# Kernel tuning notes

Hardware: AMD Instinct MI355X
Metric: run time of the kernel (lower is better)

The kernel has to match this reference:

```python
import jax, jax.numpy as jnp
import numpy as np

DEPTH = 6; HEADS = 6; DIM = 384; HD = DIM // HEADS
WS = 14; WINDOW_BLOCKS = (0, 1, 3, 4)
IMG = 512; PATCH = 16; GRID = IMG // PATCH        # 32x32 token grid
PRE_GRID = 14                                      # 224 // 16 pretrain grid
SCALE = HD ** -0.5


def layer_norm(x, w, b, eps=1e-5):
    u = x.mean(-1, keepdims=True)
    s = ((x - u) ** 2).mean(-1, keepdims=True)
    return (x - u) / jnp.sqrt(s + eps) * w + b


def get_rel_pos(size, rel_pos):
    # q_size == k_size here; relative coords in [0, 2*size-2]
    coords = jnp.arange(size)[:, None] - jnp.arange(size)[None, :] + (size - 1)
    return rel_pos[coords]  # (size, size, HD)


def attention(x, qkv_w, qkv_b, proj_w, proj_b, rel_h, rel_w):
    B, H, W, C = x.shape
    N = H * W
    qkv = (x.reshape(B, N, C) @ qkv_w.T + qkv_b).reshape(B, N, 3, HEADS, HD)
    qkv = jnp.moveaxis(qkv, 2, 0).transpose(0, 1, 3, 2, 4)  # (3,B,h,N,d)
    q, k, v = qkv[0], qkv[1], qkv[2]
    attn = jnp.einsum('bhqd,bhkd->bhqk', q * SCALE, k)
    # decomposed relative position bias (ViTDet add_decomposed_rel_pos)
    Rh = get_rel_pos(H, rel_h)  # (H,H,d)
    Rw = get_rel_pos(W, rel_w)  # (W,W,d)
    rq = q.reshape(B, HEADS, H, W, HD)
    bias_h = jnp.einsum('bnhwc,hkc->bnhwk', rq, Rh)  # (B,h,H,W,H)
    bias_w = jnp.einsum('bnhwc,wkc->bnhwk', rq, Rw)  # (B,h,H,W,W)
    attn = (attn.reshape(B, HEADS, H, W, H, W)
            + bias_h[..., :, None] + bias_w[..., None, :]).reshape(B, HEADS, N, N)
    attn = jax.nn.softmax(attn, axis=-1)
    out = jnp.einsum('bhqk,bhkd->bhqd', attn, v)
    out = out.transpose(0, 2, 1, 3).reshape(B, H, W, C)
    return out @ proj_w.T + proj_b


def window_partition(x, ws):
    B, H, W, C = x.shape
    pad_h = (ws - H % ws) % ws
    pad_w = (ws - W % ws) % ws
    x = jnp.pad(x, ((0, 0), (0, pad_h), (0, pad_w), (0, 0)))
    Hp, Wp = H + pad_h, W + pad_w
    x = x.reshape(B, Hp // ws, ws, Wp // ws, ws, C)
    x = x.transpose(0, 1, 3, 2, 4, 5).reshape(-1, ws, ws, C)
    return x, Hp, Wp


def window_unpartition(win, ws, Hp, Wp, H, W):
    B = win.shape[0] // ((Hp // ws) * (Wp // ws))
    x = win.reshape(B, Hp // ws, Wp // ws, ws, ws, -1)
    x = x.transpose(0, 1, 3, 2, 4, 5).reshape(B, Hp, Wp, -1)
    return x[:, :H, :W]


def block(x, p, windowed):
    shortcut = x
    x = layer_norm(x, p['n1w'], p['n1b'])
    if windowed:
        H, W = x.shape[1], x.shape[2]
        x, Hp, Wp = window_partition(x, WS)
    x = attention(x, p['qw'], p['qb'], p['pw'], p['pb'], p['rh'], p['rw'])
    if windowed:
        x = window_unpartition(x, WS, Hp, Wp, H, W)
    x = shortcut + x
    h = layer_norm(x, p['n2w'], p['n2b'])
    h = jax.nn.gelu(h @ p['f1w'].T + p['f1b'], approximate=False)
    return x + h @ p['f2w'].T + p['f2b']


def vit_forward(x, patch_w, patch_b, pos_embed, norm1_w, norm1_b, qkv_w, qkv_b,
                proj_w, proj_b, norm2_w, norm2_b, fc1_w, fc1_b, fc2_w, fc2_b,
                rel_pos_h, rel_pos_w):
    y = jax.lax.conv_general_dilated(
        x, patch_w, (PATCH, PATCH), 'VALID',
        dimension_numbers=('NCHW', 'OIHW', 'NCHW'))
    y = y.transpose(0, 2, 3, 1) + patch_b  # (B, GRID, GRID, DIM)
    # abs pos embed: bicubic resize from pretrain 14x14 grid to 32x32
    pos = pos_embed.reshape(1, PRE_GRID, PRE_GRID, DIM)
    pos = jax.image.resize(pos, (1, GRID, GRID, DIM), 'bicubic')
    y = y + pos
    for i in range(DEPTH):
        windowed = i in WINDOW_BLOCKS
        L = 2 * WS - 1 if windowed else 2 * GRID - 1
        p = dict(n1w=norm1_w[i], n1b=norm1_b[i], qw=qkv_w[i], qb=qkv_b[i],
                 pw=proj_w[i], pb=proj_b[i], rh=rel_pos_h[i, :L], rw=rel_pos_w[i, :L],
                 n2w=norm2_w[i], n2b=norm2_b[i], f1w=fc1_w[i], f1b=fc1_b[i],
                 f2w=fc2_w[i], f2b=fc2_b[i])
        y = block(y, p, windowed)
    return y.transpose(0, 3, 1, 2)  # (B, DIM, GRID, GRID) 'last_feat'


def setup_inputs() -> dict:
    key = jax.random.key(0)
    ks = jax.random.split(key, 10)
    B = 4
    std = 0.02
    f32 = jnp.float32
    return {
        'x': jax.random.normal(ks[0], (B, 3, IMG, IMG), f32),
        'patch_w': jax.random.normal(ks[1], (DIM, 3, PATCH, PATCH), f32) * 0.05,
        'patch_b': jnp.zeros((DIM,), f32),
        'pos_embed': jax.random.normal(ks[2], (1, PRE_GRID * PRE_GRID, DIM), f32) * std,
        'norm1_w': jnp.ones((DEPTH, DIM), f32),
        'norm1_b': jnp.zeros((DEPTH, DIM), f32),
        'qkv_w': jax.random.normal(ks[3], (DEPTH, 3 * DIM, DIM), f32) * std,
        'qkv_b': jnp.zeros((DEPTH, 3 * DIM), f32),
        'proj_w': jax.random.normal(ks[4], (DEPTH, DIM, DIM), f32) * std,
        'proj_b': jnp.zeros((DEPTH, DIM), f32),
        'norm2_w': jnp.ones((DEPTH, DIM), f32),
        'norm2_b': jnp.zeros((DEPTH, DIM), f32),
        'fc1_w': jax.random.normal(ks[5], (DEPTH, 4 * DIM, DIM), f32) * std,
        'fc1_b': jnp.zeros((DEPTH, 4 * DIM), f32),
        'fc2_w': jax.random.normal(ks[6], (DEPTH, DIM, 4 * DIM), f32) * std,
        'fc2_b': jnp.zeros((DEPTH, DIM), f32),
        'rel_pos_h': jax.random.normal(ks[7], (DEPTH, 2 * GRID - 1, HD), f32) * std,
        'rel_pos_w': jax.random.normal(ks[8], (DEPTH, 2 * GRID - 1, HD), f32) * std,
    }


def reference(x, patch_w, patch_b, pos_embed, norm1_w, norm1_b, qkv_w, qkv_b,
              proj_w, proj_b, norm2_w, norm2_b, fc1_w, fc1_b, fc2_w, fc2_b,
              rel_pos_h, rel_pos_w):
    return vit_forward(x, patch_w, patch_b, pos_embed, norm1_w, norm1_b, qkv_w, qkv_b,
                       proj_w, proj_b, norm2_w, norm2_b, fc1_w, fc1_b, fc2_w, fc2_b,
                       rel_pos_h, rel_pos_w)
```

## Files before the change

### kernel.cpp

```cpp
#include <hip/hip_runtime.h>
#include <hip/hip_bf16.h>
#include <math.h>

#define B_SZ 4
#define DIM 384
#define HEADS 6
#define HD 64
#define NTOK 4096
#define WS 14
#define NWIN 36
#define WTOK 196

typedef unsigned short u16;
typedef __bf16 bf16_t;
typedef bf16_t bf16x8 __attribute__((ext_vector_type(8)));
typedef float f32x4 __attribute__((ext_vector_type(4)));

__device__ __forceinline__ float bf2f(unsigned u) { return __uint_as_float(u << 16); }
__device__ __forceinline__ u16 f2bf(float f) {
    unsigned u = __float_as_uint(f);
    unsigned r = (u + 0x7fffu + ((u >> 16) & 1u)) >> 16;
    return (u16)r;
}
__device__ __forceinline__ unsigned pk2bf(float a, float b) {
    __hip_bfloat162 h = __float22bfloat162_rn(make_float2(a, b));
    unsigned r; __builtin_memcpy(&r, &h, 4); return r;
}

__device__ __forceinline__ void ldsload16(const u16* g, u16* l) {
    __builtin_amdgcn_global_load_lds(
        (const __attribute__((address_space(1))) unsigned int*)g,
        (__attribute__((address_space(3))) unsigned int*)l, 16, 0, 0);
}

__device__ __forceinline__ int swz(int r) { return (r ^ (r >> 2)) & 3; }

__device__ inline float cubic_keys(float x) {
    x = fabsf(x);
    if (x <= 1.f) return ((1.5f * x - 2.5f) * x) * x + 1.f;
    if (x < 2.f)  return ((-0.5f * x + 2.5f) * x - 4.f) * x + 2.f;
    return 0.f;
}

__global__ __launch_bounds__(256) void setup_kernel(
        const float* __restrict__ p0, const float* __restrict__ p1,
        const float* __restrict__ p2, const float* __restrict__ p3,
        const float* __restrict__ p4, const float* __restrict__ p5,
        u16* __restrict__ wb, const float* __restrict__ pe,
        float* __restrict__ posr, const float* __restrict__ x,
        u16* __restrict__ col) {
    int i = (blockIdx.x * 256 + threadIdx.x) * 4;
    if (i < 10918656) {
        const float* s; int off;
        if      (i <   294912) { s = p0; off = 0; }
        else if (i <  2949120) { s = p1; off = 294912; }
        else if (i <  3833856) { s = p2; off = 2949120; }
        else if (i <  7372800) { s = p3; off = 3833856; }
        else if (i < 10911744) { s = p4; off = 7372800; }
        else                   { s = p5; off = 10911744; }
        float4 v = *(const float4*)(s + (i - off));
        u16 o[4] = { f2bf(v.x), f2bf(v.y), f2bf(v.z), f2bf(v.w) };
        *(uint2*)(wb + i) = *(const uint2*)o;
        return;
    }
    i -= 10918656;
    if (i < 393216) {
        int c = i % 384;
        int g = i / 384;
        int gy = g / 32, gx = g % 32;
        float wy[14], wx[14];
        float sy = (gy + 0.5f) * (14.f / 32.f) - 0.5f;
        float sx = (gx + 0.5f) * (14.f / 32.f) - 0.5f;
        float toty = 0.f, totx = 0.f;
        #pragma unroll
        for (int k = 0; k < 14; ++k) {
            wy[k] = cubic_keys(sy - (float)k); toty += wy[k];
            wx[k] = cubic_keys(sx - (float)k); totx += wx[k];
        }
        float4 acc = {0.f, 0.f, 0.f, 0.f};
        #pragma unroll 1
        for (int iy = 0; iy < 14; ++iy) {
            if (wy[iy] == 0.f) continue;
            float4 row = {0.f, 0.f, 0.f, 0.f};
            for (int ix = 0; ix < 14; ++ix) {
                if (wx[ix] == 0.f) continue;
                float4 pv = *(const float4*)(pe + (iy * 14 + ix) * 384 + c);
                row.x += wx[ix] * pv.x; row.y += wx[ix] * pv.y;
                row.z += wx[ix] * pv.z; row.w += wx[ix] * pv.w;
            }
            acc.x += wy[iy] * row.x; acc.y += wy[iy] * row.y;
            acc.z += wy[iy] * row.z; acc.w += wy[iy] * row.w;
        }
        float inv = 1.f / (toty * totx);
        acc.x *= inv; acc.y *= inv; acc.z *= inv; acc.w *= inv;
        *(float4*)(posr + i) = acc;
        return;
    }
    i -= 393216;
    if (i < 3145728) {
        int kk = i % 768;
        int p  = i / 768;
        int b  = p / 1024;
        int ph = (p % 1024) / 32;
        int pw = p % 32;
        int c = kk / 256;
        int r = kk % 256;
        int ii = r / 16, j = r % 16;
        float4 v = *(const float4*)(x + (size_t)b * 3 * 512 * 512 +
                                    (size_t)c * 512 * 512 +
                                    (size_t)(ph * 16 + ii) * 512 + (pw * 16 + j));
        u16 o[4] = { f2bf(v.x), f2bf(v.y), f2bf(v.z), f2bf(v.w) };
        *(uint2*)(col + i) = *(const uint2*)o;
    }
}

__global__ __launch_bounds__(256) void ln_kernel(const float* __restrict__ y,
        const float* __restrict__ lw, const float* __restrict__ lb,
        u16* __restrict__ lnout)
{
    int tok = blockIdx.x * 4 + (threadIdx.x >> 6);
    int t = threadIdx.x & 63;
    size_t base = (size_t)tok * 384;
    float v[6];
    float s = 0.f;
    #pragma unroll
    for (int i = 0; i < 6; ++i) {
        v[i] = y[base + t + 64 * i]; s += v[i];
    }
    #pragma unroll
    for (int off = 32; off > 0; off >>= 1) s += __shfl_xor(s, off);
    float mean = s * (1.f / 384.f);
    float vs = 0.f;
    #pragma unroll
    for (int i = 0; i < 6; ++i) { float d = v[i] - mean; vs += d * d; }
    #pragma unroll
    for (int off = 32; off > 0; off >>= 1) vs += __shfl_xor(vs, off);
    float inv = rsqrtf(vs * (1.f / 384.f) + 1e-5f);
    u16* orow = lnout + base;
    #pragma unroll
    for (int i = 0; i < 6; ++i) {
        int c = t + 64 * i;
        orow[c] = f2bf((v[i] - mean) * inv * lw[c] + lb[c]);
    }
}

__global__ __launch_bounds__(256) void out_transpose(const float* __restrict__ y,
        float* __restrict__ outT)
{
    __shared__ float T[64][65];
    int c0 = blockIdx.x * 64, m0 = blockIdx.y * 64;
    int t = threadIdx.x;
    int cl = t & 63, wv = t >> 6;
    #pragma unroll
    for (int r = 0; r < 16; ++r) {
        int ml = wv * 16 + r;
        T[ml][cl] = y[(size_t)(m0 + ml) * 384 + c0 + cl];
    }
    __syncthreads();
    int b = m0 >> 10, g0 = m0 & 1023;
    int gl = t & 63;
    #pragma unroll
    for (int r = 0; r < 16; ++r) {
        int ccl = wv * 16 + r;
        outT[((size_t)(b * 384 + c0 + ccl)) * 1024 + g0 + gl] = T[gl][ccl];
    }
}

__global__ __launch_bounds__(256) void mfma_gemm4(
        const u16* __restrict__ A, const u16* __restrict__ Wt,
        const float* __restrict__ bias,
        u16* __restrict__ outb,
        int M, int N, int K, int act)
{
    __shared__ u16 As[2][8192];
    __shared__ u16 Bs[2][4096];
    int t = threadIdx.x;
    int lane = t & 63, wave = t >> 6;
    int wm = (wave >> 1) * 64, wn = (wave & 1) * 32;
    int m0 = blockIdx.y * 128, n0 = blockIdx.x * 64;

    int r0 = t >> 2,        c0 = ((t & 3) ^ swz(t >> 2)) * 8;
    int r1 = 64 + (t >> 2), c1 = ((t & 3) ^ swz(64 + (t >> 2))) * 8;
    const u16* a0 = A + (size_t)(m0 + r0) * K + c0;
    const u16* a1 = A + (size_t)(m0 + r1) * K + c1;
    const u16* b0 = Wt + (size_t)(n0 + r0) * K + c0;

    auto stage = [&](int k0, int buf) {
        ldsload16(a0 + k0,      &As[buf][wave * 512]);
        ldsload16(a1 + k0,      &As[buf][2048 + wave * 512]);
        ldsload16(b0 + k0,      &Bs[buf][wave * 512]);
        ldsload16(a0 + k0 + 32, &As[buf][4096 + wave * 512]);
        ldsload16(a1 + k0 + 32, &As[buf][6144 + wave * 512]);
        ldsload16(b0 + k0 + 32, &Bs[buf][2048 + wave * 512]);
    };

    f32x4 acc[4][2] = {};
    int row_a = wm + (lane & 15);
    int row_b = wn + (lane & 15);
    int lq = lane >> 4;
    int nchunks = K / 64;

    stage(0, 0);
    __syncthreads();

    for (int ci = 0; ci < nchunks; ++ci) {
        int p = ci & 1;
        bool pref = (ci + 1 < nchunks);
        if (pref) stage((ci + 1) * 64, 1 - p);
        #pragma unroll
        for (int hf = 0; hf < 2; ++hf) {
            bf16x8 af[4], bfr[2];
            #pragma unroll
            for (int i = 0; i < 4; ++i) {
                int r = row_a + i * 16;
                af[i] = *(const bf16x8*)&As[p][hf * 4096 + r * 32 + ((lq ^ swz(r)) * 8)];
            }
            #pragma unroll
            for (int j = 0; j < 2; ++j) {
                int r = row_b + j * 16;
                bfr[j] = *(const bf16x8*)&Bs[p][hf * 2048 + r * 32 + ((lq ^ swz(r)) * 8)];
            }
            #pragma unroll
            for (int i = 0; i < 4; ++i)
                #pragma unroll
                for (int j = 0; j < 2; ++j)
                    acc[i][j] = __builtin_amdgcn_mfma_f32_16x16x32_bf16(
                        af[i], bfr[j], acc[i][j], 0, 0, 0);
        }
        if (pref) __syncthreads();
    }

    int colq = lane & 15, rowq = (lane >> 4) * 4;
    #pragma unroll
    for (int i = 0; i < 4; ++i) {
        #pragma unroll
        for (int rr = 0; rr < 4; ++rr) {
            int m = m0 + wm + i * 16 + rowq + rr;
            size_t mo = (size_t)m * N;
            #pragma unroll
            for (int j = 0; j < 2; ++j) {
                int n = n0 + wn + j * 16 + colq;
                float v = acc[i][j][rr] + bias[n];
                if (act)  v = 0.5f * v * (1.f + erff(v * 0.70710678118654752f));
                outb[mo + n] = f2bf(v);
            }
        }
    }
}

__global__ __launch_bounds__(256) void mfma_gemm32(
        const u16* __restrict__ A, const u16* __restrict__ Wt,
        const float* __restrict__ bias, const float* __restrict__ posr,
        float* __restrict__ y, int addy, int M, int N, int K)
{
    __shared__ u16 As[2][4096];
    __shared__ u16 Bs[2][2048];
    int t = threadIdx.x;
    int lane = t & 63, wave = t >> 6;
    int wm = (wave >> 1) * 32, wn = (wave & 1) * 16;
    int m0 = blockIdx.y * 64, n0 = blockIdx.x * 32;

    int r0 = t >> 2, c0 = ((t & 3) ^ swz(t >> 2)) * 8;
    const u16* a0 = A + (size_t)(m0 + r0) * K + c0;
    int tb = t & 127;
    int rb = tb >> 2, cb = ((tb & 3) ^ swz(tb >> 2)) * 8;
    const u16* b0 = Wt + (size_t)(n0 + rb) * K + cb;

    auto stage = [&](int k0, int buf) {
        ldsload16(a0 + k0,      &As[buf][wave * 512]);
        ldsload16(a0 + k0 + 32, &As[buf][2048 + wave * 512]);
        if (wave < 2) ldsload16(b0 + k0,      &Bs[buf][wave * 512]);
        else          ldsload16(b0 + k0 + 32, &Bs[buf][1024 + (wave - 2) * 512]);
    };

    f32x4 acc[2] = {};
    int row_a = wm + (lane & 15);
    int row_b = wn + (lane & 15);
    int lq = lane >> 4;
    int nchunks = K / 64;

    stage(0, 0);
    __syncthreads();

    for (int ci = 0; ci < nchunks; ++ci) {
        int p = ci & 1;
        bool pref = (ci + 1 < nchunks);
        if (pref) stage((ci + 1) * 64, 1 - p);
        #pragma unroll
        for (int hf = 0; hf < 2; ++hf) {
            bf16x8 af[2], bf0;
            #pragma unroll
            for (int i = 0; i < 2; ++i) {
                int r = row_a + i * 16;
                af[i] = *(const bf16x8*)&As[p][hf * 2048 + r * 32 + ((lq ^ swz(r)) * 8)];
            }
            {
                int r = row_b;
                bf0 = *(const bf16x8*)&Bs[p][hf * 1024 + r * 32 + ((lq ^ swz(r)) * 8)];
            }
            #pragma unroll
            for (int i = 0; i < 2; ++i)
                acc[i] = __builtin_amdgcn_mfma_f32_16x16x32_bf16(
                    af[i], bf0, acc[i], 0, 0, 0);
        }
        if (pref) __syncthreads();
    }

    int colq = lane & 15, rowq = (lane >> 4) * 4;
    #pragma unroll
    for (int i = 0; i < 2; ++i) {
        #pragma unroll
        for (int rr = 0; rr < 4; ++rr) {
            int m = m0 + wm + i * 16 + rowq + rr;
            size_t mo = (size_t)m * N;
            int n = n0 + wn + colq;
            float v = acc[i][rr] + bias[n];
            if (posr) v += posr[(size_t)(m & 1023) * 384 + n];
            if (addy) v += y[mo + n];
            y[mo + n] = v;
        }
    }
}

__global__ __launch_bounds__(256) void mfma_gemm32b(
        const u16* __restrict__ A, const u16* __restrict__ Wt,
        const float* __restrict__ bias, u16* __restrict__ outb,
        int M, int N, int K)
{
    __shared__ u16 As[2][4096];
    __shared__ u16 Bs[2][2048];
    int t = threadIdx.x;
    int lane = t & 63, wave = t >> 6;
    int wm = (wave >> 1) * 32, wn = (wave & 1) * 16;
    int m0 = blockIdx.y * 64, n0 = blockIdx.x * 32;

    int r0 = t >> 2, c0 = ((t & 3) ^ swz(t >> 2)) * 8;
    const u16* a0 = A + (size_t)(m0 + r0) * K + c0;
    int tb = t & 127;
    int rb = tb >> 2, cb = ((tb & 3) ^ swz(tb >> 2)) * 8;
    const u16* b0 = Wt + (size_t)(n0 + rb) * K + cb;

    auto stage = [&](int k0, int buf) {
        ldsload16(a0 + k0,      &As[buf][wave * 512]);
        ldsload16(a0 + k0 + 32, &As[buf][2048 + wave * 512]);
        if (wave < 2) ldsload16(b0 + k0,      &Bs[buf][wave * 512]);
        else          ldsload16(b0 + k0 + 32, &Bs[buf][1024 + (wave - 2) * 512]);
    };

    f32x4 acc[2] = {};
    int row_a = wm + (lane & 15);
    int row_b = wn + (lane & 15);
    int lq = lane >> 4;
    int nchunks = K / 64;

    stage(0, 0);
    __syncthreads();

    for (int ci = 0; ci < nchunks; ++ci) {
        int p = ci & 1;
        bool pref = (ci + 1 < nchunks);
        if (pref) stage((ci + 1) * 64, 1 - p);
        #pragma unroll
        for (int hf = 0; hf < 2; ++hf) {
            bf16x8 af[2], bf0;
            #pragma unroll
            for (int i = 0; i < 2; ++i) {
                int r = row_a + i * 16;
                af[i] = *(const bf16x8*)&As[p][hf * 2048 + r * 32 + ((lq ^ swz(r)) * 8)];
            }
            {
                int r = row_b;
                bf0 = *(const bf16x8*)&Bs[p][hf * 1024 + r * 32 + ((lq ^ swz(r)) * 8)];
            }
            #pragma unroll
            for (int i = 0; i < 2; ++i)
                acc[i] = __builtin_amdgcn_mfma_f32_16x16x32_bf16(
                    af[i], bf0, acc[i], 0, 0, 0);
        }
        if (pref) __syncthreads();
    }

    int colq = lane & 15, rowq = (lane >> 4) * 4;
    #pragma unroll
    for (int i = 0; i < 2; ++i) {
        #pragma unroll
        for (int rr = 0; rr < 4; ++rr) {
            int m = m0 + wm + i * 16 + rowq + rr;
            size_t mo = (size_t)m * N;
            int n = n0 + wn + colq;
            outb[mo + n] = f2bf(acc[i][rr] + bias[n]);
        }
    }
}

template<int N, int W>
__global__ __launch_bounds__(256) void attn_mfma(const u16* __restrict__ qkv,
        const u16* __restrict__ qkb, const float* __restrict__ rh,
        const float* __restrict__ rw, u16* __restrict__ outb,
        float* __restrict__ opart, float* __restrict__ lpart)
{
    constexpr int JS = (W == 32) ? 64 : 32;
    constexpr int L  = (W == 32) ? 63 : 27;
    constexpr int CTR = W - 1;
    constexpr int KSPAN = (W == 32) ? 512 : 224;
    constexpr int NKT = KSPAN / 32;
    __shared__ u16 KV[11776];
    __shared__ u16 bhl[64 * 66];
    __shared__ u16 bwl[64 * 66];
    __shared__ u16 Qt[64 * 66];
    __shared__ unsigned kofs[224];

    u16* Pb = KV + 9216;
    u16* Rt = KV;

    int t = threadIdx.x, lane = t & 63, wave = t >> 6;
    int quad = lane >> 4, l15 = lane & 15;
    int uh = blockIdx.x, qb0 = blockIdx.y * 64;
    int z = (W == 32) ? blockIdx.z : 0;
    int kstart = z * KSPAN;
    int h = uh % HEADS, u = uh / HEADS;
    size_t tbase = (size_t)u * 1024;
    int wb_ = u / 9, wr = u - wb_ * 9;
    int wy = wr / 3, wx = wr - wy * 3;

    auto tok14 = [&](int iy, int ix) -> const u16* {
        int gy = wy * WS + iy, gx = wx * WS + ix;
        if (gy < 32 && gx < 32)
            return qkv + (size_t)(wb_ * 1024 + gy * 32 + gx) * 1152;
        return qkb;
    };
    auto rowptr = [&](int lq2) -> const u16* {
        if constexpr (W == 32) {
            return qkv + (tbase + lq2) * 1152;
        } else {
            int iy = lq2 / WS, ix = lq2 - iy * WS;
            return tok14(iy, ix);
        }
    };

    {
        int q = t & 63, ch0 = (t >> 6) * 16;
        int qc = qb0 + q; if (qc >= N) qc = N - 1;
        const u16* qp = rowptr(qc) + h * 64 + ch0;
        uint4 a = *(const uint4*)qp;
        uint4 b = *(const uint4*)(qp + 8);
        u16 vals[16];
        *(uint4*)vals = a; *(uint4*)(vals + 8) = b;
        #pragma unroll
        for (int c = 0; c < 16; ++c)
            Qt[(ch0 + c) * 66 + q] = ((qb0 + q) < N) ? vals[c] : (u16)0;
    }

    if constexpr (W != 32) {
        if (t < 224) {
            int kh = t / WS;
            kofs[t] = (unsigned)kh | ((unsigned)(t - kh * WS) << 16);
        }
    }

    for (int idx = t; idx < JS * 16; idx += 256) {
        int table = (idx >= JS * 8) ? 1 : 0;
        int id2 = idx & (JS * 8 - 1);
        int j = id2 >> 3, cc0 = (id2 & 7) * 8;
        const float* tab = table ? rw : rh;
        u16 tmp[8];
        if (j < L) {
            const float* src = tab + (size_t)j * 64 + cc0;
            #pragma unroll
            for (int c = 0; c < 8; ++c) tmp[c] = f2bf(src[c]);
        } else {
            #pragma unroll
            for (int c = 0; c < 8; ++c) tmp[c] = 0;
        }
        *(uint4*)&Rt[table * JS * 72 + j * 72 + cc0] = *(uint4*)tmp;
    }
    __syncthreads();

    {
        int tb0 = (W == 32) ? 0 : (wave >> 1);
        int ntb = (W == 32) ? 2 : 1;
        int jt  = (W == 32) ? wave : (wave & 1);
        for (int tt = 0; tt < ntb; ++tt) {
            int table = tb0 + tt;
            const u16* Rtt = Rt + table * JS * 72;
            bf16x8 af0 = *(const bf16x8*)&Rtt[(jt * 16 + l15) * 72 + quad * 8];
            bf16x8 af1 = *(const bf16x8*)&Rtt[(jt * 16 + l15) * 72 + 32 + quad * 8];
            u16* dst = table ? bwl : bhl;
            #pragma unroll
            for (int qt = 0; qt < 4; ++qt) {
                bf16x8 qf0, qf1;
                u16* p0 = (u16*)&qf0; u16* p1 = (u16*)&qf1;
                #pragma unroll
                for (int zz = 0; zz < 8; ++zz) {
                    p0[zz] = Qt[(quad * 8 + zz) * 66 + qt * 16 + l15];
                    p1[zz] = Qt[(32 + quad * 8 + zz) * 66 + qt * 16 + l15];
                }
                f32x4 acc = {};
                acc = __builtin_amdgcn_mfma_f32_16x16x32_bf16(af0, qf0, acc, 0, 0, 0);
                acc = __builtin_amdgcn_mfma_f32_16x16x32_bf16(af1, qf1, acc, 0, 0, 0);
                #pragma unroll
                for (int r = 0; r < 4; ++r)
                    dst[(qt * 16 + l15) * 66 + jt * 16 + quad * 4 + r] = f2bf(acc[r]);
            }
        }
    }
    __syncthreads();

    int skey = (wave * 64 + lane) >> 3;
    int sc8  = ((wave * 64 + lane) & 7) ^ (skey & 7);
    int vkey = t & 31, vch0 = (t >> 5) * 8;
    int siy = 0, six = 0, viy = 0, vix = 0;
    if constexpr (W != 32) {
        int k0 = kstart + skey;
        siy = k0 / WS; six = k0 - siy * WS;
        int k1 = kstart + vkey;
        viy = k1 / WS; vix = k1 - viy * WS;
    }
    auto adv = [](int& iy, int& ix) { ix += 4; iy += 2; if (ix >= WS) { ix -= WS; ++iy; } };

    {
        const u16* kp = (W == 32) ? qkv + (tbase + kstart + skey) * 1152
                                  : tok14(siy, six);
        ldsload16(kp + 384 + h * 64 + sc8 * 8, KV + wave * 512);
        const u16* vp = (W == 32) ? qkv + (tbase + kstart + vkey) * 1152
                                  : tok14(viy, vix);
        uint4 vv = *(const uint4*)(vp + 768 + h * 64 + vch0);
        u16 tmp[8]; *(uint4*)tmp = vv;
        u16* vdst = KV + 4096;
        #pragma unroll
        for (int c = 0; c < 8; ++c) vdst[(vch0 + c) * 40 + vkey] = tmp[c];
        if constexpr (W != 32) { adv(siy, six); adv(viy, vix); }
    }

    bf16x8 qf[2];
    #pragma unroll
    for (int hc = 0; hc < 2; ++hc) {
        u16* qv = (u16*)&qf[hc];
        #pragma unroll
        for (int j = 0; j < 8; ++j)
            qv[j] = Qt[(hc * 32 + quad * 8 + j) * 66 + wave * 16 + l15];
    }
    int qme = wave * 16 + l15;
    bool wactive = (W == 32) ? true : ((qb0 + wave * 16) < N);
    int qq = qb0 + qme; if (qq >= N) qq = N - 1;
    int qh = qq / W, qw = qq - qh * W;
    int qh13 = qh + CTR, qw13 = qw + CTR;
    float bwreg[2][4];
    if constexpr (W == 32) {
        #pragma unroll
        for (int kc2 = 0; kc2 < 2; ++kc2)
            #pragma unroll
            for (int r = 0; r < 4; ++r) {
                int keyl = kc2 * 16 + quad * 4 + r;
                bwreg[kc2][r] = bf2f(bwl[qme * 66 + (qw - keyl + CTR)]);
            }
    }

    f32x4 of[4] = {};
    float lsum = 0.f;
    __syncthreads();

    for (int kt = 0; kt < NKT; ++kt) {
        int kb = kstart + kt * 32;
        int p = kt & 1;
        const u16* ksp = KV + p * 2048;
        const u16* vtp = KV + 4096 + p * 2560;
        bool pref = (kt + 1 < NKT);
        uint4 vpref;
        if (pref) {
            const u16* kp = (W == 32) ? qkv + (tbase + kb + 32 + skey) * 1152
                                      : tok14(siy, six);
            ldsload16(kp + 384 + h * 64 + sc8 * 8, KV + (1 - p) * 2048 + wave * 512);
            const u16* vp = (W == 32) ? qkv + (tbase + kb + 32 + vkey) * 1152
                                      : tok14(viy, vix);
            vpref = *(const uint4*)(vp + 768 + h * 64 + vch0);
            if constexpr (W != 32) { adv(siy, six); adv(viy, vix); }
        }

        if (wactive) {
            f32x4 st[2] = {};
            #pragma unroll
            for (int hc = 0; hc < 2; ++hc) {
                #pragma unroll
                for (int kc2 = 0; kc2 < 2; ++kc2) {
                    int key = kc2 * 16 + l15;
                    int c8 = hc * 4 + quad;
                    int pp = key * 8 + (c8 ^ (key & 7));
                    bf16x8 kf = *(const bf16x8*)&ksp[pp * 8];
                    st[kc2] = __builtin_amdgcn_mfma_f32_16x16x32_bf16(
                        kf, qf[hc], st[kc2], 0, 0, 0);
                }
            }
            float bh_t = 0.f;
            if constexpr (W == 32) bh_t = bf2f(bhl[qme * 66 + (qh - (kb >> 5) + CTR)]);
            #pragma unroll
            for (int kc2 = 0; kc2 < 2; ++kc2) {
                float pv4[4];
                #pragma unroll
                for (int r = 0; r < 4; ++r) {
                    int keyl = kc2 * 16 + quad * 4 + r;
                    float pv;
                    if constexpr (W == 32) {
                        float b = bh_t + bwreg[kc2][r];
                        pv = __expf(fmaf(st[kc2][r], 0.125f, b));
                    } else {
                        unsigned ko = kofs[kb + keyl];
                        float b = bf2f(bhl[qme * 66 + qh13 - (int)(ko & 0xffffu)]) +
                                  bf2f(bwl[qme * 66 + qw13 - (int)(ko >> 16)]);
                        pv = __expf(fmaf(st[kc2][r], 0.125f, b));
                        if (kb + keyl >= N) pv = 0.f;
                    }
                    lsum += pv;
                    pv4[r] = pv;
                }
                uint2 pk;
                pk.x = pk2bf(pv4[0], pv4[1]);
                pk.y = pk2bf(pv4[2], pv4[3]);
                *(uint2*)&Pb[wave * 640 + l15 * 40 + kc2 * 16 + quad * 4] = pk;
            }
            bf16x8 pf = *(const bf16x8*)&Pb[wave * 640 + l15 * 40 + quad * 8];
            #pragma unroll
            for (int ca = 0; ca < 4; ++ca) {
                bf16x8 vf = *(const bf16x8*)&vtp[(ca * 16 + l15) * 40 + quad * 8];
                of[ca] = __builtin_amdgcn_mfma_f32_16x16x32_bf16(
                    vf, pf, of[ca], 0, 0, 0);
            }
        }

        if (pref) {
            u16 tmp[8]; *(uint4*)tmp = vpref;
            u16* vdst = KV + 4096 + (1 - p) * 2560;
            #pragma unroll
            for (int c = 0; c < 8; ++c) vdst[(vch0 + c) * 40 + vkey] = tmp[c];
            __syncthreads();
        }
    }

    lsum += __shfl_xor(lsum, 16);
    lsum += __shfl_xor(lsum, 32);
    int q = qb0 + qme;
    if constexpr (W == 32) {
        size_t ridx = (size_t)z * 24576 + (size_t)uh * 1024 + q;
        float* op = opart + ridx * 64;
        #pragma unroll
        for (int ca = 0; ca < 4; ++ca)
            *(float4*)&op[ca * 16 + quad * 4] = (float4){of[ca][0], of[ca][1],
                                                         of[ca][2], of[ca][3]};
        if (quad == 0) lpart[ridx] = lsum;
    } else {
        float inv = 1.f / lsum;
        if (q < N) {
            int iy = q / WS, ix = q - iy * WS;
            int gy = wy * WS + iy, gx = wx * WS + ix;
            if (gy >= 32 || gx >= 32) return;
            u16* op = outb + (size_t)(wb_ * 1024 + gy * 32 + gx) * 384 + h * 64;
            #pragma unroll
            for (int ca = 0; ca < 4; ++ca) {
                uint2 pk;
                pk.x = pk2bf(of[ca][0] * inv, of[ca][1] * inv);
                pk.y = pk2bf(of[ca][2] * inv, of[ca][3] * inv);
                *(uint2*)&op[ca * 16 + quad * 4] = pk;
            }
        }
    }
}

__global__ __launch_bounds__(256) void attn_merge_kernel(const float* __restrict__ O,
        const float* __restrict__ Lp, u16* __restrict__ attb)
{
    int gi = blockIdx.x * 256 + threadIdx.x;
    int idx = gi >> 4;
    int ch = (gi & 15) * 4;
    float4 o0 = *(const float4*)&O[(size_t)idx * 64 + ch];
    float4 o1 = *(const float4*)&O[((size_t)24576 + idx) * 64 + ch];
    float inv = 1.f / (Lp[idx] + Lp[24576 + idx]);
    int uh = idx >> 10, q = idx & 1023;
    int u = uh / 6, h = uh - u * 6;
    uint2 pk;
    pk.x = pk2bf((o0.x + o1.x) * inv, (o0.y + o1.y) * inv);
    pk.y = pk2bf((o0.z + o1.z) * inv, (o0.w + o1.w) * inv);
    *(uint2*)(attb + ((size_t)(u * 1024 + q)) * 384 + h * 64 + ch) = pk;
}

static inline void launch_gemm(const u16* A, const u16* W, const float* bias,
                               u16* outb, int M, int N, int K, int act,
                               hipStream_t s) {
    dim3 g(N / 64, M / 128, 1);
    mfma_gemm4<<<g, 256, 0, s>>>(A, W, bias, outb, M, N, K, act);
}

static inline void launch_gemm32(const u16* A, const u16* W, const float* bias,
                                 const float* posr, float* y, int addy,
                                 int M, int N, int K, hipStream_t s) {
    dim3 g(N / 32, M / 64, 1);
    mfma_gemm32<<<g, 256, 0, s>>>(A, W, bias, posr, y, addy, M, N, K);
}

static inline void launch_gemm32b(const u16* A, const u16* W, const float* bias,
                                  u16* outb, int M, int N, int K, hipStream_t s) {
    dim3 g(N / 32, M / 64, 1);
    mfma_gemm32b<<<g, 256, 0, s>>>(A, W, bias, outb, M, N, K);
}

extern "C" void kernel_launch(void* const* d_in, const int* in_sizes, int n_in,
                              void* d_out, int out_size, void* d_ws, size_t ws_size,
                              hipStream_t stream) {
    const float* x      = (const float*)d_in[0];
    const float* patchw = (const float*)d_in[1];
    const float* patchb = (const float*)d_in[2];
    const float* pos    = (const float*)d_in[3];
    const float* n1w    = (const float*)d_in[4];
    const float* n1b    = (const float*)d_in[5];
    const float* qkvw   = (const float*)d_in[6];
    const float* qkvb   = (const float*)d_in[7];
    const float* pw     = (const float*)d_in[8];
    const float* pb     = (const float*)d_in[9];
    const float* n2w    = (const float*)d_in[10];
    const float* n2b    = (const float*)d_in[11];
    const float* f1w    = (const float*)d_in[12];
    const float* f1b    = (const float*)d_in[13];
    const float* f2w    = (const float*)d_in[14];
    const float* f2b    = (const float*)d_in[15];
    const float* rph    = (const float*)d_in[16];
    const float* rpw    = (const float*)d_in[17];
    float* out = (float*)d_out;

    float* y   = (float*)d_ws;
    u16* attb  = (u16*)(y + 1572864);
    u16* mlpb  = attb + 1572864;
    u16* lnb   = mlpb + 6291456;
    u16* qkvx  = lnb + 1572864;
    u16* rsrv  = qkvx + 4718592;
    u16* wb    = rsrv + 7864320;
    float* posr = (float*)(wb + 10918656);

    u16* colb  = rsrv;
    float* Opart   = (float*)mlpb;
    float* Lpart   = (float*)lnb;

    u16* wb_patch = wb;
    u16* wb_qkv   = wb + 294912;
    u16* wb_pw    = wb + 2949120;
    u16* wb_f1    = wb + 3833856;
    u16* wb_f2    = wb + 7372800;
    u16* wqb      = wb + 10911744;

    setup_kernel<<<(14457600 / 4 + 255) / 256, 256, 0, stream>>>(
        patchw, qkvw, pw, f1w, f2w, qkvb, wb, pos, posr, x, colb);

    launch_gemm32(colb, wb_patch, patchb, posr, y, 0, NTOK, 384, 768, stream);
    ln_kernel<<<1024, 256, 0, stream>>>(y, n1w, n1b, lnb);

    for (int i = 0; i < 6; ++i) {
        bool windowed = (i == 0 || i == 1 || i == 3 || i == 4);
        const float* rh = rph + (size_t)i * 63 * 64;
        const float* rw = rpw + (size_t)i * 63 * 64;
        launch_gemm32b(lnb, wb_qkv + (size_t)i * 442368, qkvb + i * 1152,
                       qkvx, NTOK, 1152, 384, stream);
        if (windowed) {
            attn_mfma<WTOK, WS><<<dim3(NWIN * HEADS, 4, 1), 256, 0, stream>>>(
                qkvx, wqb + i * 1152, rh, rw, attb, nullptr, nullptr);
        } else {
            attn_mfma<1024, 32><<<dim3(B_SZ * HEADS, 16, 2), 256, 0, stream>>>(
                qkvx, wqb + i * 1152, rh, rw, nullptr, Opart, Lpart);
            attn_merge_kernel<<<1536, 256, 0, stream>>>(Opart, Lpart, attb);
        }
        launch_gemm32(attb, wb_pw + (size_t)i * 147456, pb + i * 384,
                      nullptr, y, 1, NTOK, 384, 384, stream);
        ln_kernel<<<1024, 256, 0, stream>>>(y, n2w + i * 384, n2b + i * 384, lnb);
        launch_gemm(lnb, wb_f1 + (size_t)i * 589824, f1b + i * 1536,
                    mlpb, NTOK, 1536, 384, 1, stream);
        launch_gemm32(mlpb, wb_f2 + (size_t)i * 589824, f2b + i * 384,
                      nullptr, y, 1, NTOK, 384, 1536, stream);
        if (i < 5)
            ln_kernel<<<1024, 256, 0, stream>>>(y, n1w + (i + 1) * 384,
                                                n1b + (i + 1) * 384, lnb);
        else
            out_transpose<<<dim3(6, 64), 256, 0, stream>>>(y, out);
    }
}
```

Measured before the change: 684.1 us.

## Remap GEMM blocks across XCDs, widen QKV tile, deepen K-chunk in gemm32

```diff
diff --git a/kernel.cpp b/kernel.cpp
--- a/kernel.cpp
+++ b/kernel.cpp
@@ -34,6 +34,18 @@
 }
 
 __device__ __forceinline__ int swz(int r) { return (r ^ (r >> 2)) & 3; }
+
+__device__ __forceinline__ void xcd_remap(int& bx, int& by) {
+    int nwg = gridDim.x * gridDim.y;
+    int id = blockIdx.y * gridDim.x + blockIdx.x;
+    if ((nwg & 7) == 0) {
+        int nid = (id & 7) * (nwg >> 3) + (id >> 3);
+        by = nid / gridDim.x;
+        bx = nid - by * gridDim.x;
+    } else {
+        bx = blockIdx.x; by = blockIdx.y;
+    }
+}
 
 __device__ inline float cubic_keys(float x) {
     x = fabsf(x);
@@ -177,7 +189,9 @@
     int t = threadIdx.x;
     int lane = t & 63, wave = t >> 6;
     int wm = (wave >> 1) * 64, wn = (wave & 1) * 32;
-    int m0 = blockIdx.y * 128, n0 = blockIdx.x * 64;
+    int bx, by;
+    xcd_remap(bx, by);
+    int m0 = by * 128, n0 = bx * 64;
 
     int r0 = t >> 2,        c0 = ((t & 3) ^ swz(t >> 2)) * 8;
     int r1 = 64 + (t >> 2), c1 = ((t & 3) ^ swz(64 + (t >> 2))) * 8;
@@ -248,17 +262,96 @@
     }
 }
 
+__global__ __launch_bounds__(256) void mfma_gemm64b(
+        const u16* __restrict__ A, const u16* __restrict__ Wt,
+        const float* __restrict__ bias, u16* __restrict__ outb,
+        int M, int N, int K)
+{
+    __shared__ u16 As[2][4096];
+    __shared__ u16 Bs[2][4096];
+    int t = threadIdx.x;
+    int lane = t & 63, wave = t >> 6;
+    int wm = (wave >> 1) * 32, wn = (wave & 1) * 32;
+    int bx, by;
+    xcd_remap(bx, by);
+    int m0 = by * 64, n0 = bx * 64;
+
+    int r0 = t >> 2, c0 = ((t & 3) ^ swz(t >> 2)) * 8;
+    const u16* a0 = A + (size_t)(m0 + r0) * K + c0;
+    const u16* b0 = Wt + (size_t)(n0 + r0) * K + c0;
+
+    auto stage = [&](int k0, int buf) {
+        ldsload16(a0 + k0,      &As[buf][wave * 512]);
+        ldsload16(b0 + k0,      &Bs[buf][wave * 512]);
+        ldsload16(a0 + k0 + 32, &As[buf][2048 + wave * 512]);
+        ldsload16(b0 + k0 + 32, &Bs[buf][2048 + wave * 512]);
+    };
+
+    f32x4 acc[2][2] = {};
+    int row_a = wm + (lane & 15);
+    int row_b = wn + (lane & 15);
+    int lq = lane >> 4;
+    int nchunks = K / 64;
+
+    stage(0, 0);
+    __syncthreads();
+
+    for (int ci = 0; ci < nchunks; ++ci) {
+        int p = ci & 1;
+        bool pref = (ci + 1 < nchunks);
+        if (pref) stage((ci + 1) * 64, 1 - p);
+        #pragma unroll
+        for (int hf = 0; hf < 2; ++hf) {
+            bf16x8 af[2], bfr[2];
+            #pragma unroll
+            for (int i = 0; i < 2; ++i) {
+                int r = row_a + i * 16;
+                af[i] = *(const bf16x8*)&As[p][hf * 2048 + r * 32 + ((lq ^ swz(r)) * 8)];
+            }
+            #pragma unroll
+            for (int j = 0; j < 2; ++j) {
+                int r = row_b + j * 16;
+                bfr[j] = *(const bf16x8*)&Bs[p][hf * 2048 + r * 32 + ((lq ^ swz(r)) * 8)];
+            }
+            #pragma unroll
+            for (int i = 0; i < 2; ++i)
+                #pragma unroll
+                for (int j = 0; j < 2; ++j)
+                    acc[i][j] = __builtin_amdgcn_mfma_f32_16x16x32_bf16(
+                        af[i], bfr[j], acc[i][j], 0, 0, 0);
+        }
+        if (pref) __syncthreads();
+    }
+
+    int colq = lane & 15, rowq = (lane >> 4) * 4;
+    #pragma unroll
+    for (int i = 0; i < 2; ++i) {
+        #pragma unroll
+        for (int rr = 0; rr < 4; ++rr) {
+            int m = m0 + wm + i * 16 + rowq + rr;
+            size_t mo = (size_t)m * N;
+            #pragma unroll
+            for (int j = 0; j < 2; ++j) {
+                int n = n0 + wn + j * 16 + colq;
+                outb[mo + n] = f2bf(acc[i][j][rr] + bias[n]);
+            }
+        }
+    }
+}
+
 __global__ __launch_bounds__(256) void mfma_gemm32(
         const u16* __restrict__ A, const u16* __restrict__ Wt,
         const float* __restrict__ bias, const float* __restrict__ posr,
         float* __restrict__ y, int addy, int M, int N, int K)
 {
-    __shared__ u16 As[2][4096];
-    __shared__ u16 Bs[2][2048];
+    __shared__ u16 As[2][8192];
+    __shared__ u16 Bs[2][4096];
     int t = threadIdx.x;
     int lane = t & 63, wave = t >> 6;
     int wm = (wave >> 1) * 32, wn = (wave & 1) * 16;
-    int m0 = blockIdx.y * 64, n0 = blockIdx.x * 32;
+    int bx, by;
+    xcd_remap(bx, by);
+    int m0 = by * 64, n0 = bx * 32;
 
     int r0 = t >> 2, c0 = ((t & 3) ^ swz(t >> 2)) * 8;
     const u16* a0 = A + (size_t)(m0 + r0) * K + c0;
@@ -269,15 +362,22 @@
     auto stage = [&](int k0, int buf) {
         ldsload16(a0 + k0,      &As[buf][wave * 512]);
         ldsload16(a0 + k0 + 32, &As[buf][2048 + wave * 512]);
-        if (wave < 2) ldsload16(b0 + k0,      &Bs[buf][wave * 512]);
-        else          ldsload16(b0 + k0 + 32, &Bs[buf][1024 + (wave - 2) * 512]);
+        ldsload16(a0 + k0 + 64, &As[buf][4096 + wave * 512]);
+        ldsload16(a0 + k0 + 96, &As[buf][6144 + wave * 512]);
+        if (wave < 2) {
+            ldsload16(b0 + k0,      &Bs[buf][wave * 512]);
+            ldsload16(b0 + k0 + 64, &Bs[buf][2048 + wave * 512]);
+        } else {
+            ldsload16(b0 + k0 + 32, &Bs[buf][1024 + (wave - 2) * 512]);
+            ldsload16(b0 + k0 + 96, &Bs[buf][3072 + (wave - 2) * 512]);
+        }
     };
 
     f32x4 acc[2] = {};
     int row_a = wm + (lane & 15);
     int row_b = wn + (lane & 15);
     int lq = lane >> 4;
-    int nchunks = K / 64;
+    int nchunks = K / 128;
 
     stage(0, 0);
     __syncthreads();
@@ -285,9 +385,9 @@
     for (int ci = 0; ci < nchunks; ++ci) {
         int p = ci & 1;
         bool pref = (ci + 1 < nchunks);
-        if (pref) stage((ci + 1) * 64, 1 - p);
-        #pragma unroll
-        for (int hf = 0; hf < 2; ++hf) {
+        if (pref) stage((ci + 1) * 128, 1 - p);
+        #pragma unroll
+        for (int hf = 0; hf < 4; ++hf) {
             bf16x8 af[2], bf0;
             #pragma unroll
             for (int i = 0; i < 2; ++i) {
@@ -318,77 +418,6 @@
             if (posr) v += posr[(size_t)(m & 1023) * 384 + n];
             if (addy) v += y[mo + n];
             y[mo + n] = v;
-        }
-    }
-}
-
-__global__ __launch_bounds__(256) void mfma_gemm32b(
-        const u16* __restrict__ A, const u16* __restrict__ Wt,
-        const float* __restrict__ bias, u16* __restrict__ outb,
-        int M, int N, int K)
-{
-    __shared__ u16 As[2][4096];
-    __shared__ u16 Bs[2][2048];
-    int t = threadIdx.x;
-    int lane = t & 63, wave = t >> 6;
-    int wm = (wave >> 1) * 32, wn = (wave & 1) * 16;
-    int m0 = blockIdx.y * 64, n0 = blockIdx.x * 32;
-
-    int r0 = t >> 2, c0 = ((t & 3) ^ swz(t >> 2)) * 8;
-    const u16* a0 = A + (size_t)(m0 + r0) * K + c0;
-    int tb = t & 127;
-    int rb = tb >> 2, cb = ((tb & 3) ^ swz(tb >> 2)) * 8;
-    const u16* b0 = Wt + (size_t)(n0 + rb) * K + cb;
-
-    auto stage = [&](int k0, int buf) {
-        ldsload16(a0 + k0,      &As[buf][wave * 512]);
-        ldsload16(a0 + k0 + 32, &As[buf][2048 + wave * 512]);
-        if (wave < 2) ldsload16(b0 + k0,      &Bs[buf][wave * 512]);
-        else          ldsload16(b0 + k0 + 32, &Bs[buf][1024 + (wave - 2) * 512]);
-    };
-
-    f32x4 acc[2] = {};
-    int row_a = wm + (lane & 15);
-    int row_b = wn + (lane & 15);
-    int lq = lane >> 4;
-    int nchunks = K / 64;
-
-    stage(0, 0);
-    __syncthreads();
-
-    for (int ci = 0; ci < nchunks; ++ci) {
-        int p = ci & 1;
-        bool pref = (ci + 1 < nchunks);
-        if (pref) stage((ci + 1) * 64, 1 - p);
-        #pragma unroll
-        for (int hf = 0; hf < 2; ++hf) {
-            bf16x8 af[2], bf0;
-            #pragma unroll
-            for (int i = 0; i < 2; ++i) {
-                int r = row_a + i * 16;
-                af[i] = *(const bf16x8*)&As[p][hf * 2048 + r * 32 + ((lq ^ swz(r)) * 8)];
-            }
-            {
-                int r = row_b;
-                bf0 = *(const bf16x8*)&Bs[p][hf * 1024 + r * 32 + ((lq ^ swz(r)) * 8)];
-            }
-            #pragma unroll
-            for (int i = 0; i < 2; ++i)
-                acc[i] = __builtin_amdgcn_mfma_f32_16x16x32_bf16(
-                    af[i], bf0, acc[i], 0, 0, 0);
-        }
-        if (pref) __syncthreads();
-    }
-
-    int colq = lane & 15, rowq = (lane >> 4) * 4;
-    #pragma unroll
-    for (int i = 0; i < 2; ++i) {
-        #pragma unroll
-        for (int rr = 0; rr < 4; ++rr) {
-            int m = m0 + wm + i * 16 + rowq + rr;
-            size_t mo = (size_t)m * N;
-            int n = n0 + wn + colq;
-            outb[mo + n] = f2bf(acc[i][rr] + bias[n]);
         }
     }
 }
@@ -689,17 +718,17 @@
     mfma_gemm4<<<g, 256, 0, s>>>(A, W, bias, outb, M, N, K, act);
 }
 
+static inline void launch_gemm64b(const u16* A, const u16* W, const float* bias,
+                                  u16* outb, int M, int N, int K, hipStream_t s) {
+    dim3 g(N / 64, M / 64, 1);
+    mfma_gemm64b<<<g, 256, 0, s>>>(A, W, bias, outb, M, N, K);
+}
+
 static inline void launch_gemm32(const u16* A, const u16* W, const float* bias,
                                  const float* posr, float* y, int addy,
                                  int M, int N, int K, hipStream_t s) {
     dim3 g(N / 32, M / 64, 1);
     mfma_gemm32<<<g, 256, 0, s>>>(A, W, bias, posr, y, addy, M, N, K);
-}
-
-static inline void launch_gemm32b(const u16* A, const u16* W, const float* bias,
-                                  u16* outb, int M, int N, int K, hipStream_t s) {
-    dim3 g(N / 32, M / 64, 1);
-    mfma_gemm32b<<<g, 256, 0, s>>>(A, W, bias, outb, M, N, K);
 }
 
 extern "C" void kernel_launch(void* const* d_in, const int* in_sizes, int n_in,
@@ -755,7 +784,7 @@
         bool windowed = (i == 0 || i == 1 || i == 3 || i == 4);
         const float* rh = rph + (size_t)i * 63 * 64;
         const float* rw = rpw + (size_t)i * 63 * 64;
-        launch_gemm32b(lnb, wb_qkv + (size_t)i * 442368, qkvb + i * 1152,
+        launch_gemm64b(lnb, wb_qkv + (size_t)i * 442368, qkvb + i * 1152,
                        qkvx, NTOK, 1152, 384, stream);
         if (windowed) {
             attn_mfma<WTOK, WS><<<dim3(NWIN * HEADS, 4, 1), 256, 0, stream>>>(
```

After: 641.9 us, median of 3. -6.2%, faster.
